# Performance work log

Hardware: AMD Instinct MI355X
Metric: run time of the kernel (lower is better)

Reference implementation:

```python
import jax, jax.numpy as jnp
import numpy as np

N_NODES = 100000
N_EDGES = 1600000
N_GRAPHS = 64
IN_DIM = 128
HID = 64
N_CLASSES = 10


def setup_inputs() -> dict:
    key = jax.random.key(0)
    ks = jax.random.split(key, 8)
    x = jax.random.normal(ks[0], (N_NODES, IN_DIM), jnp.float32)
    edge_index = jax.random.randint(ks[1], (2, N_EDGES), 0, N_NODES, jnp.int32)
    graph_id = jnp.sort(jax.random.randint(ks[2], (N_NODES,), 0, N_GRAPHS, jnp.int32))
    W1 = jax.random.normal(ks[3], (IN_DIM, HID), jnp.float32) / np.sqrt(IN_DIM)
    b1 = jnp.zeros((HID,), jnp.float32)
    W2 = jax.random.normal(ks[4], (HID, HID), jnp.float32) / np.sqrt(HID)
    b2 = jnp.zeros((HID,), jnp.float32)
    attn_W = jax.random.normal(ks[5], (HID, 1), jnp.float32) / np.sqrt(HID)
    attn_b = jnp.zeros((1,), jnp.float32)
    cls_W = jax.random.normal(ks[6], (HID, N_CLASSES), jnp.float32) / np.sqrt(HID)
    cls_b = jnp.zeros((N_CLASSES,), jnp.float32)
    return {"x": x, "edge_index": edge_index, "graph_id": graph_id,
            "W1": W1, "b1": b1, "W2": W2, "b2": b2,
            "attn_W": attn_W, "attn_b": attn_b, "cls_W": cls_W, "cls_b": cls_b}


def _graph_conv(h, W, b, src, dst, norm_out, norm_in):
    # DGL GraphConv, norm='both': D_in^{-1/2} A D_out^{-1/2} (h W) + b
    h = h @ W                                  # [N, out]
    h = h * norm_out[:, None]                  # scale by src out-degree^{-1/2}
    m = jax.ops.segment_sum(h[src], dst, num_segments=N_NODES)  # SpMM aggregation
    return m * norm_in[:, None] + b


def reference(x, edge_index, graph_id, W1, b1, W2, b2, attn_W, attn_b, cls_W, cls_b):
    src, dst = edge_index[0], edge_index[1]
    ones_e = jnp.ones((src.shape[0],), jnp.float32)
    deg_out = jnp.clip(jax.ops.segment_sum(ones_e, src, num_segments=N_NODES), 1.0)
    deg_in = jnp.clip(jax.ops.segment_sum(ones_e, dst, num_segments=N_NODES), 1.0)
    norm_out = jax.lax.rsqrt(deg_out)
    norm_in = jax.lax.rsqrt(deg_in)

    h = jax.nn.relu(_graph_conv(x, W1, b1, src, dst, norm_out, norm_in))
    h = jax.nn.relu(_graph_conv(h, W2, b2, src, dst, norm_out, norm_in))

    hw = jax.nn.sigmoid(h @ attn_W + attn_b)   # [N, 1] attention gate
    h = h * hw

    # mean_nodes: per-graph mean pooling
    sums = jax.ops.segment_sum(h, graph_id, num_segments=N_GRAPHS)        # [G, HID]
    cnts = jnp.clip(jax.ops.segment_sum(jnp.ones((N_NODES,), jnp.float32), graph_id,
                                        num_segments=N_GRAPHS), 1.0)
    hg = sums / cnts[:, None]
    out = hg @ cls_W + cls_b                   # [G, n_classes]
    return out, hw
```

## Files before the change

kernel.cpp:

```cpp
#include <hip/hip_runtime.h>
#include <stdint.h>


#define N_NODES   100000
#define N_EDGES   1600000
#define N_GRAPHS  64
#define IN_DIM    128
#define HID       64
#define N_CLASSES 10

#define NBUCK     391
#define P1B       196
#define EPB       8192
#define GB_BLOCKS 391
#define MTILES    6250
#define GEMM_BLOCKS 1563
#define NSLOT     (NBUCK * 256)
#define SPMM_BLOCKS 3128
#define POOL_SLICES 32
#define WS_NEED   33885952u

typedef __attribute__((ext_vector_type(8))) short short8v;
typedef __attribute__((ext_vector_type(4))) float f32x4;
typedef __bf16 bf16x8 __attribute__((ext_vector_type(8)));

__device__ __forceinline__ f32x4 mfma16(short8v a, short8v b, f32x4 c) {
  return __builtin_amdgcn_mfma_f32_16x16x32_bf16(
      __builtin_bit_cast(bf16x8, a), __builtin_bit_cast(bf16x8, b), c, 0, 0, 0);
}

__device__ __forceinline__ float bf2f(unsigned short u) {
  unsigned int v = ((unsigned int)u) << 16;
  float f;
  __builtin_memcpy(&f, &v, 4);
  return f;
}

__device__ __forceinline__ unsigned short f2bf(float f) {
  unsigned int x;
  __builtin_memcpy(&x, &f, 4);
  unsigned int lsb = (x >> 16) & 1u;
  x += 0x7fffu + lsb;
  return (unsigned short)(x >> 16);
}

__device__ __forceinline__ void unpack_bf2(unsigned int u, float& lo, float& hi) {
  unsigned int a = u << 16;
  unsigned int b = u & 0xffff0000u;
  __builtin_memcpy(&lo, &a, 4);
  __builtin_memcpy(&hi, &b, 4);
}

__device__ __forceinline__ float ldf(const void* p, int i, int mode) {
  return mode ? bf2f(((const unsigned short*)p)[i]) : ((const float*)p)[i];
}

__global__ __launch_bounds__(256) void fallback_kernel(unsigned short* __restrict__ out,
                                                       int n) {
  int i = blockIdx.x * 256 + threadIdx.x;
  if (i < n) out[i] = 0;
}

__global__ __launch_bounds__(256) void wcvt_kernel(
    const unsigned short* __restrict__ xu,
    const void* __restrict__ W1, const void* __restrict__ W2,
    const void* __restrict__ b1, const void* __restrict__ b2,
    const void* __restrict__ attnW, const void* __restrict__ attnb,
    const void* __restrict__ clsW, const void* __restrict__ clsb,
    unsigned short* __restrict__ W1hf, unsigned short* __restrict__ W1lf,
    unsigned short* __restrict__ W2hf, unsigned short* __restrict__ W2lf,
    float* __restrict__ b1f, float* __restrict__ b2f,
    float* __restrict__ attnWf, float* __restrict__ attnbf,
    float* __restrict__ clsWf, float* __restrict__ clsbf,
    int* __restrict__ flag) {
  __shared__ int cnt[4];
  __shared__ int smode;
  int tid = (int)threadIdx.x;
  unsigned u = xu[2 * tid];
  int e = (int)((u >> 7) & 0xFF);
  int ok = (e >= 110 && e <= 132) ? 1 : 0;
  unsigned long long m = __ballot(ok);
  if ((tid & 63) == 0) cnt[tid >> 6] = __popcll(m);
  __syncthreads();
  if (tid == 0) {
    smode = (cnt[0] + cnt[1] + cnt[2] + cnt[3] > 128) ? 1 : 0;
    if (blockIdx.x == 0) {
      flag[0] = smode;
      flag[1] = 1;
    }
  }
  __syncthreads();
  int mode = smode;

  int i = blockIdx.x * 256 + tid;
  if (i < 1024) {
    int tile = i >> 6, lane = i & 63;
    int kt = tile >> 2, ct = tile & 3;
#pragma unroll
    for (int j = 0; j < 8; ++j) {
      int k = kt * 32 + ((lane >> 4) << 3) + j;
      int d = (ct << 4) + (lane & 15);
      float v = ldf(W1, k * HID + d, mode);
      unsigned short h = f2bf(v);
      unsigned short l = f2bf(v - bf2f(h));
      W1hf[i * 8 + j] = h;
      W1lf[i * 8 + j] = l;
    }
  } else if (i < 1536) {
    int ii = i - 1024;
    int tile = ii >> 6, lane = ii & 63;
    int kt = tile >> 2, ct = tile & 3;
#pragma unroll
    for (int j = 0; j < 8; ++j) {
      int k = kt * 32 + ((lane >> 4) << 3) + j;
      int d = (ct << 4) + (lane & 15);
      float v = ldf(W2, k * HID + d, mode);
      unsigned short h = f2bf(v);
      unsigned short l = f2bf(v - bf2f(h));
      W2hf[ii * 8 + j] = h;
      W2lf[ii * 8 + j] = l;
    }
  }
  if (i < HID) {
    b1f[i] = ldf(b1, i, mode);
    b2f[i] = ldf(b2, i, mode);
    attnWf[i] = ldf(attnW, i, mode);
  }
  if (i == 0) attnbf[0] = ldf(attnb, 0, mode);
  if (i < HID * N_CLASSES) clsWf[i] = ldf(clsW, i, mode);
  if (i < N_CLASSES) clsbf[i] = ldf(clsb, i, mode);
}

template <int K, bool SCALE>
__device__ __forceinline__ void gemm_tile(
    const void* __restrict__ A, const unsigned short* __restrict__ Whf,
    const unsigned short* __restrict__ Wlf, const float* __restrict__ norm_out,
    unsigned short* __restrict__ out, int mode, int mtile, int lane) {
  int n0 = mtile << 4;
  int row = lane & 15;
  int kg = lane >> 4;
  f32x4 acc0 = {0.f, 0.f, 0.f, 0.f};
  f32x4 acc1 = {0.f, 0.f, 0.f, 0.f};
  f32x4 acc2 = {0.f, 0.f, 0.f, 0.f};
  f32x4 acc3 = {0.f, 0.f, 0.f, 0.f};
  const short8v* whb0 = (const short8v*)Whf + lane;
  const short8v* wlb0 = (const short8v*)Wlf + lane;
  if (mode) {
    const unsigned short* xr = (const unsigned short*)A + (size_t)(n0 + row) * K + (kg << 3);
#pragma unroll
    for (int kt = 0; kt < K / 32; ++kt) {
      uint4 va = *(const uint4*)(xr + kt * 32);
      short8v xh = __builtin_bit_cast(short8v, va);
      const short8v* wh = whb0 + (size_t)(kt * 4) * 64;
      const short8v* wl = wlb0 + (size_t)(kt * 4) * 64;
      acc0 = mfma16(xh, wh[0], acc0);
      acc1 = mfma16(xh, wh[64], acc1);
      acc2 = mfma16(xh, wh[128], acc2);
      acc3 = mfma16(xh, wh[192], acc3);
      acc0 = mfma16(xh, wl[0], acc0);
      acc1 = mfma16(xh, wl[64], acc1);
      acc2 = mfma16(xh, wl[128], acc2);
      acc3 = mfma16(xh, wl[192], acc3);
    }
  } else {
    const float* xr = (const float*)A + (size_t)(n0 + row) * K + (kg << 3);
#pragma unroll
    for (int kt = 0; kt < K / 32; ++kt) {
      float4 a0 = *(const float4*)(xr + kt * 32);
      float4 a1 = *(const float4*)(xr + kt * 32 + 4);
      float xv[8] = {a0.x, a0.y, a0.z, a0.w, a1.x, a1.y, a1.z, a1.w};
      short8v xh, xl;
#pragma unroll
      for (int j = 0; j < 8; ++j) {
        unsigned short h = f2bf(xv[j]);
        unsigned short l = f2bf(xv[j] - bf2f(h));
        xh[j] = (short)h;
        xl[j] = (short)l;
      }
      const short8v* wh = whb0 + (size_t)(kt * 4) * 64;
      const short8v* wl = wlb0 + (size_t)(kt * 4) * 64;
      acc0 = mfma16(xh, wh[0], acc0);
      acc1 = mfma16(xh, wh[64], acc1);
      acc2 = mfma16(xh, wh[128], acc2);
      acc3 = mfma16(xh, wh[192], acc3);
      acc0 = mfma16(xh, wl[0], acc0);
      acc1 = mfma16(xh, wl[64], acc1);
      acc2 = mfma16(xh, wl[128], acc2);
      acc3 = mfma16(xh, wl[192], acc3);
      acc0 = mfma16(xl, wh[0], acc0);
      acc1 = mfma16(xl, wh[64], acc1);
      acc2 = mfma16(xl, wh[128], acc2);
      acc3 = mfma16(xl, wh[192], acc3);
    }
  }
  int col = lane & 15;
#pragma unroll
  for (int i = 0; i < 4; ++i) {
    int n = n0 + (kg << 2) + i;
    float s = SCALE ? norm_out[n] : 1.f;
    size_t rb = (size_t)n << 6;
    out[rb + col]      = f2bf(acc0[i] * s);
    out[rb + 16 + col] = f2bf(acc1[i] * s);
    out[rb + 32 + col] = f2bf(acc2[i] * s);
    out[rb + 48 + col] = f2bf(acc3[i] * s);
  }
}

__global__ __launch_bounds__(256) void fatA_kernel(
    const int* __restrict__ ei, int* __restrict__ blkhistD,
    int* __restrict__ blkhistS,
    const int* __restrict__ gid, int* __restrict__ gstart,
    const void* __restrict__ x, const unsigned short* __restrict__ W1hf,
    const unsigned short* __restrict__ W1lf, unsigned short* __restrict__ bufA,
    const int* __restrict__ flag) {
  int b = (int)blockIdx.x;
  int t = (int)threadIdx.x;
  if (b < P1B) {
    __shared__ int hD[NBUCK];
    __shared__ int hS[NBUCK];
    for (int i = t; i < NBUCK; i += 256) { hD[i] = 0; hS[i] = 0; }
    __syncthreads();
    int base_e = b * EPB;
    for (int s = 0; s < EPB / 1024; ++s) {
      int e4 = base_e + s * 1024 + t * 4;
      if (e4 < N_EDGES) {
        int4 s4 = *(const int4*)(ei + e4);
        int4 d4 = *(const int4*)(ei + N_EDGES + e4);
        int ss[4] = {s4.x, s4.y, s4.z, s4.w};
        int dd[4] = {d4.x, d4.y, d4.z, d4.w};
#pragma unroll
        for (int j = 0; j < 4; ++j) {
          if ((unsigned)ss[j] < N_NODES) atomicAdd(&hS[ss[j] >> 8], 1);
          if ((unsigned)dd[j] < N_NODES) atomicAdd(&hD[dd[j] >> 8], 1);
        }
      }
    }
    __syncthreads();
    for (int i = t; i < NBUCK; i += 256) {
      blkhistD[i * P1B + b] = hD[i];
      blkhistS[i * P1B + b] = hS[i];
    }
  } else if (b < P1B + GEMM_BLOCKS) {
    int mode = flag[0];
    int mtile = (b - P1B) * 4 + (t >> 6);
    if (mtile < MTILES)
      gemm_tile<IN_DIM, false>(x, W1hf, W1lf, (const float*)0, bufA, mode,
                               mtile, t & 63);
  } else {
    int bb = b - P1B - GEMM_BLOCKS;
    int n = bb * 256 + t;
    if (n >= N_NODES) return;
    int gc = gid[n] & (N_GRAPHS - 1);
    if (n == 0) {
      for (int g = 0; g <= gc; ++g) gstart[g] = 0;
    } else {
      int gp = gid[n - 1] & (N_GRAPHS - 1);
      for (int g = gp + 1; g <= gc; ++g) gstart[g] = n;
    }
    if (n == N_NODES - 1) {
      for (int g = gc + 1; g <= N_GRAPHS; ++g) gstart[g] = N_NODES;
    }
  }
}

__global__ __launch_bounds__(512) void bucket_tot_kernel(
    const int* __restrict__ blkhistD, const int* __restrict__ blkhistS,
    int* __restrict__ bstart_d, int* __restrict__ bstart_s) {
  const int* hist = (blockIdx.x == 0) ? blkhistD : blkhistS;
  int* bst  = (blockIdx.x == 0) ? bstart_d : bstart_s;
  int u = (int)threadIdx.x;
  int tot = 0;
  if (u < NBUCK) {
    const int* row = hist + u * P1B;
    for (int blk = 0; blk < P1B; ++blk) tot += row[blk];
  }
  __shared__ int smA[512];
  __shared__ int smB[512];
  smA[u] = tot;
  __syncthreads();
  int* a = smA;
  int* bq = smB;
  for (int off = 1; off < 512; off <<= 1) {
    int v = a[u];
    if (u >= off) v += a[u - off];
    bq[u] = v;
    __syncthreads();
    int* tmp = a; a = bq; bq = tmp;
  }
  int excl = a[u] - tot;
  if (u <= NBUCK) bst[u] = excl;
}

__global__ __launch_bounds__(256) void bucket_base_kernel(
    int* __restrict__ blkhistD, int* __restrict__ blkhistS,
    const int* __restrict__ bstart_d, const int* __restrict__ bstart_s) {
  int bb = (int)blockIdx.x;
  int* hist = (bb < NBUCK) ? blkhistD : blkhistS;
  const int* bst = (bb < NBUCK) ? bstart_d : bstart_s;
  int u = (bb < NBUCK) ? bb : bb - NBUCK;
  int t = (int)threadIdx.x;
  int h = (t < P1B) ? hist[u * P1B + t] : 0;
  __shared__ int smA[256];
  __shared__ int smB[256];
  smA[t] = h;
  __syncthreads();
  int* a = smA;
  int* bq = smB;
  for (int off = 1; off < 256; off <<= 1) {
    int v = a[t];
    if (t >= off) v += a[t - off];
    bq[t] = v;
    __syncthreads();
    int* tmp = a; a = bq; bq = tmp;
  }
  int excl = a[t] - h;
  if (t < P1B) hist[u * P1B + t] = bst[u] + excl;
}

__global__ __launch_bounds__(256) void part_scatter_kernel(
    const int* __restrict__ ei, const int* __restrict__ blkbaseD,
    const int* __restrict__ blkbaseS,
    unsigned int* __restrict__ edstP, int* __restrict__ esrc) {
  __shared__ int cD[NBUCK];
  __shared__ int cS[NBUCK];
  int b = (int)blockIdx.x;
  int t = (int)threadIdx.x;
  for (int i = t; i < NBUCK; i += 256) {
    cD[i] = blkbaseD[i * P1B + b];
    cS[i] = blkbaseS[i * P1B + b];
  }
  __syncthreads();
  int base_e = b * EPB;
  for (int s = 0; s < EPB / 1024; ++s) {
    int e4 = base_e + s * 1024 + t * 4;
    if (e4 < N_EDGES) {
      int4 s4 = *(const int4*)(ei + e4);
      int4 d4 = *(const int4*)(ei + N_EDGES + e4);
      int ss[4] = {s4.x, s4.y, s4.z, s4.w};
      int dd[4] = {d4.x, d4.y, d4.z, d4.w};
#pragma unroll
      for (int j = 0; j < 4; ++j) {
        if ((unsigned)ss[j] < N_NODES) {
          int slot = atomicAdd(&cS[ss[j] >> 8], 1);
          esrc[slot] = ss[j];
        }
        if ((unsigned)dd[j] < N_NODES) {
          int slot = atomicAdd(&cD[dd[j] >> 8], 1);
          edstP[slot] = ((unsigned int)ss[j] << 8) | ((unsigned int)dd[j] & 255u);
        }
      }
    }
  }
}

__global__ __launch_bounds__(256) void csr_kernel(
    const unsigned int* __restrict__ edstP, const int* __restrict__ esrc,
    const int* __restrict__ bstart_d, const int* __restrict__ bstart_s,
    int* __restrict__ rowptr, int* __restrict__ colx,
    float* __restrict__ norm_in, float* __restrict__ norm_out,
    int* __restrict__ perm) {
  __shared__ int lc[256];
  __shared__ int smA[256];
  __shared__ int smB[256];
  int b = (int)blockIdx.x;
  int t = (int)threadIdx.x;
  if (b < NBUCK) {
    int node0 = b << 8;
    int base = bstart_d[b];
    int end  = bstart_d[b + 1];
    lc[t] = 0;
    __syncthreads();
    for (int i = base + t; i < end; i += 256) {
      unsigned int p = edstP[i];
      atomicAdd(&lc[p & 255u], 1);
    }
    __syncthreads();
    int my = lc[t];
    smA[t] = my;
    __syncthreads();
    int* a = smA;
    int* bq = smB;
    for (int off = 1; off < 256; off <<= 1) {
      int v = a[t];
      if (t >= off) v += a[t - off];
      bq[t] = v;
      __syncthreads();
      int* tmp = a; a = bq; bq = tmp;
    }
    int excl = a[t] - my;
    int n = node0 + t;
    if (n <= N_NODES) rowptr[n] = base + excl;
    if (n < N_NODES) {
      int c = my < 1 ? 1 : my;
      norm_in[n] = rsqrtf((float)c);
    }
    __syncthreads();
    lc[t] = base + excl;
    __syncthreads();
    for (int i = base + t; i < end; i += 256) {
      unsigned int p = edstP[i];
      int slot = atomicAdd(&lc[p & 255u], 1);
      colx[slot] = (int)(p >> 8);
    }
    __syncthreads();
    int deg = my < 255 ? my : 255;
    lc[t] = 0;
    __syncthreads();
    atomicAdd(&lc[deg], 1);
    __syncthreads();
    int hv = lc[t];
    smA[t] = hv;
    __syncthreads();
    int* a2 = smA;
    int* b2 = smB;
    for (int off = 1; off < 256; off <<= 1) {
      int v = a2[t];
      if (t >= off) v += a2[t - off];
      b2[t] = v;
      __syncthreads();
      int* tmp = a2; a2 = b2; b2 = tmp;
    }
    int hexcl = a2[t] - hv;
    __syncthreads();
    lc[t] = hexcl;
    __syncthreads();
    int rank = atomicAdd(&lc[deg], 1);
    perm[(b << 8) + rank] = n;
  } else {
    int bb = b - NBUCK;
    int node0 = bb << 8;
    int base = bstart_s[bb];
    int end  = bstart_s[bb + 1];
    lc[t] = 0;
    __syncthreads();
    for (int i = base + t; i < end; i += 256) {
      atomicAdd(&lc[esrc[i] - node0], 1);
    }
    __syncthreads();
    int n = node0 + t;
    if (n < N_NODES) {
      int c = lc[t] < 1 ? 1 : lc[t];
      norm_out[n] = rsqrtf((float)c);
    }
  }
}

template <int K>
__global__ __launch_bounds__(256) void gemm_mfma_kernel(
    const void* __restrict__ A, const unsigned short* __restrict__ Whf,
    const unsigned short* __restrict__ Wlf, const float* __restrict__ norm_out,
    unsigned short* __restrict__ out, const int* __restrict__ flag) {
  int mode = flag[0];
  int mtile = (int)blockIdx.x * 4 + ((int)threadIdx.x >> 6);
  if (mtile >= MTILES) return;
  gemm_tile<K, true>(A, Whf, Wlf, norm_out, out, mode, mtile,
                     (int)threadIdx.x & 63);
}

__device__ __forceinline__ void accum8f(uint4 v, float no, float acc[8]) {
  float lo, hi;
  unpack_bf2(v.x, lo, hi); acc[0] = fmaf(lo, no, acc[0]); acc[1] = fmaf(hi, no, acc[1]);
  unpack_bf2(v.y, lo, hi); acc[2] = fmaf(lo, no, acc[2]); acc[3] = fmaf(hi, no, acc[3]);
  unpack_bf2(v.z, lo, hi); acc[4] = fmaf(lo, no, acc[4]); acc[5] = fmaf(hi, no, acc[5]);
  unpack_bf2(v.w, lo, hi); acc[6] = fmaf(lo, no, acc[6]); acc[7] = fmaf(hi, no, acc[7]);
}

__device__ __forceinline__ void spmm_gather8s(const unsigned short* __restrict__ hs,
                                              const int* __restrict__ col,
                                              const float* __restrict__ no,
                                              int e0, int e1, int dim0,
                                              float acc[8]) {
  int e = e0;
  for (; e + 4 <= e1; e += 4) {
    int c0 = col[e], c1 = col[e + 1], c2 = col[e + 2], c3 = col[e + 3];
    float n0 = no[c0], n1 = no[c1], n2 = no[c2], n3 = no[c3];
    uint4 v0 = *(const uint4*)(hs + ((size_t)c0 << 6) + dim0);
    uint4 v1 = *(const uint4*)(hs + ((size_t)c1 << 6) + dim0);
    uint4 v2 = *(const uint4*)(hs + ((size_t)c2 << 6) + dim0);
    uint4 v3 = *(const uint4*)(hs + ((size_t)c3 << 6) + dim0);
    accum8f(v0, n0, acc);
    accum8f(v1, n1, acc);
    accum8f(v2, n2, acc);
    accum8f(v3, n3, acc);
  }
  for (; e < e1; ++e) {
    int c = col[e];
    uint4 v = *(const uint4*)(hs + ((size_t)c << 6) + dim0);
    accum8f(v, no[c], acc);
  }
}

__device__ __forceinline__ void accum8(uint4 v, float acc[8]) {
  float lo, hi;
  unpack_bf2(v.x, lo, hi); acc[0] += lo; acc[1] += hi;
  unpack_bf2(v.y, lo, hi); acc[2] += lo; acc[3] += hi;
  unpack_bf2(v.z, lo, hi); acc[4] += lo; acc[5] += hi;
  unpack_bf2(v.w, lo, hi); acc[6] += lo; acc[7] += hi;
}

__device__ __forceinline__ void spmm_gather8(const unsigned short* __restrict__ hs,
                                             const int* __restrict__ col,
                                             int e0, int e1, int dim0,
                                             float acc[8]) {
  int e = e0;
  for (; e + 4 <= e1; e += 4) {
    int c0 = col[e], c1 = col[e + 1], c2 = col[e + 2], c3 = col[e + 3];
    uint4 v0 = *(const uint4*)(hs + ((size_t)c0 << 6) + dim0);
    uint4 v1 = *(const uint4*)(hs + ((size_t)c1 << 6) + dim0);
    uint4 v2 = *(const uint4*)(hs + ((size_t)c2 << 6) + dim0);
    uint4 v3 = *(const uint4*)(hs + ((size_t)c3 << 6) + dim0);
    accum8(v0, acc);
    accum8(v1, acc);
    accum8(v2, acc);
    accum8(v3, acc);
  }
  for (; e < e1; ++e) {
    int c = col[e];
    uint4 v = *(const uint4*)(hs + ((size_t)c << 6) + dim0);
    accum8(v, acc);
  }
}

__global__ __launch_bounds__(256) void spmm_kernel(const unsigned short* __restrict__ hs,
                                                   const int* __restrict__ rowptr,
                                                   const int* __restrict__ col,
                                                   const float* __restrict__ norm_out,
                                                   const float* __restrict__ norm_in,
                                                   const float* __restrict__ b1f,
                                                   const int* __restrict__ perm,
                                                   unsigned short* __restrict__ out) {
  int slot = (int)(blockIdx.x * 32 + (threadIdx.x >> 3));
  int n = perm[slot];
  if ((unsigned)n >= N_NODES) return;
  int dim0 = ((int)threadIdx.x & 7) << 3;
  int e0 = rowptr[n], e1 = rowptr[n + 1];
  if (e0 < 0) e0 = 0;
  if (e1 > N_EDGES) e1 = N_EDGES;
  float acc[8];
#pragma unroll
  for (int i = 0; i < 8; ++i) acc[i] = 0.f;
  spmm_gather8s(hs, col, norm_out, e0, e1, dim0, acc);
  float nin = norm_in[n];
  unsigned int pk[4];
#pragma unroll
  for (int i = 0; i < 4; ++i) {
    float vlo = fmaxf(acc[2 * i] * nin + b1f[dim0 + 2 * i], 0.f);
    float vhi = fmaxf(acc[2 * i + 1] * nin + b1f[dim0 + 2 * i + 1], 0.f);
    pk[i] = (unsigned int)f2bf(vlo) | ((unsigned int)f2bf(vhi) << 16);
  }
  *(uint4*)(out + ((size_t)n << 6) + dim0) = make_uint4(pk[0], pk[1], pk[2], pk[3]);
}

__global__ __launch_bounds__(256) void spmm_attn_kernel(
    const unsigned short* __restrict__ hs,
    const int* __restrict__ rowptr, const int* __restrict__ col,
    const float* __restrict__ norm_in, const float* __restrict__ b2f,
    const float* __restrict__ attnWf, const float* __restrict__ attnbf,
    const int* __restrict__ perm,
    void* __restrict__ out_base, unsigned short* __restrict__ gated,
    const int* __restrict__ flag) {
  int mode = flag[0];
  int slot = (int)(blockIdx.x * 32 + (threadIdx.x >> 3));
  int n = perm[slot];
  if ((unsigned)n >= N_NODES) return;
  int dim0 = ((int)threadIdx.x & 7) << 3;
  int e0 = rowptr[n], e1 = rowptr[n + 1];
  if (e0 < 0) e0 = 0;
  if (e1 > N_EDGES) e1 = N_EDGES;
  float acc[8];
#pragma unroll
  for (int i = 0; i < 8; ++i) acc[i] = 0.f;
  spmm_gather8(hs, col, e0, e1, dim0, acc);
  float nin = norm_in[n];
  float vv[8];
  float p = 0.f;
#pragma unroll
  for (int i = 0; i < 8; ++i) {
    vv[i] = fmaxf(acc[i] * nin + b2f[dim0 + i], 0.f);
    p += vv[i] * attnWf[dim0 + i];
  }
#pragma unroll
  for (int m = 1; m <= 4; m <<= 1) p += __shfl_xor(p, m, 64);
  float logit = p + attnbf[0];
  float hwv = 1.f / (1.f + __expf(-logit));
  if ((threadIdx.x & 7) == 0) {
    if (mode) ((unsigned short*)out_base)[N_GRAPHS * N_CLASSES + n] = f2bf(hwv);
    else      ((float*)out_base)[N_GRAPHS * N_CLASSES + n] = hwv;
  }
  unsigned int pk[4];
#pragma unroll
  for (int i = 0; i < 4; ++i) {
    pk[i] = (unsigned int)f2bf(vv[2 * i] * hwv) |
            ((unsigned int)f2bf(vv[2 * i + 1] * hwv) << 16);
  }
  *(uint4*)(gated + ((size_t)n << 6) + dim0) = make_uint4(pk[0], pk[1], pk[2], pk[3]);
}

__global__ __launch_bounds__(256) void pool_kernel(const unsigned short* __restrict__ gated,
                                                   const int* __restrict__ gstart,
                                                   float* __restrict__ gpart) {
  int g = (int)blockIdx.x >> 5;
  int s = (int)blockIdx.x & 31;
  int dim = (int)threadIdx.x & 63;
  int rsel = (int)threadIdx.x >> 6;
  int r0 = gstart[g], r1 = gstart[g + 1];
  if (r0 < 0) r0 = 0;
  if (r1 > N_NODES) r1 = N_NODES;
  int len = r1 - r0;
  if (len < 0) len = 0;
  int a = r0 + (int)(((long long)len * s) >> 5);
  int bnd = r0 + (int)(((long long)len * (s + 1)) >> 5);
  float acc = 0.f;
  for (int r = a + rsel; r < bnd; r += 4)
    acc += bf2f(gated[((size_t)r << 6) + dim]);
  __shared__ float sm[256];
  sm[threadIdx.x] = acc;
  __syncthreads();
  if (threadIdx.x < 64)
    gpart[((size_t)blockIdx.x << 6) + dim] =
        sm[dim] + sm[64 + dim] + sm[128 + dim] + sm[192 + dim];
}

__global__ __launch_bounds__(640) void final_kernel(const float* __restrict__ gpart,
                                                    const int* __restrict__ gstart,
                                                    const float* __restrict__ clsWf,
                                                    const float* __restrict__ clsbf,
                                                    void* __restrict__ out_base,
                                                    const int* __restrict__ flag) {
  __shared__ float gs[N_GRAPHS * HID];
  int t = (int)threadIdx.x;
  for (int idx = t; idx < N_GRAPHS * HID; idx += 640) {
    int g = idx >> 6, d = idx & 63;
    float a = 0.f;
#pragma unroll
    for (int s = 0; s < POOL_SLICES; ++s)
      a += gpart[(((size_t)(g << 5) + s) << 6) + d];
    gs[idx] = a;
  }
  __syncthreads();
  int mode = flag[0];
  if (t >= N_GRAPHS * N_CLASSES) return;
  int g = t / N_CLASSES, c = t - g * N_CLASSES;
  int cg = gstart[g + 1] - gstart[g];
  if (cg < 1) cg = 1;
  float inv = 1.f / (float)cg;
  float acc = 0.f;
#pragma unroll
  for (int d = 0; d < HID; ++d) acc += gs[(g << 6) + d] * clsWf[d * N_CLASSES + c];
  float r = acc * inv + clsbf[c];
  if (mode) ((unsigned short*)out_base)[t] = f2bf(r);
  else      ((float*)out_base)[t] = r;
}

extern "C" void kernel_launch(void* const* d_in, const int* in_sizes, int n_in,
                              void* d_out, int out_size, void* d_ws, size_t ws_size,
                              hipStream_t stream) {
  const void* x     = d_in[0];
  const int*  ei    = (const int*)d_in[1];
  const int*  gid   = (const int*)d_in[2];
  const void* W1    = d_in[3];
  const void* b1    = d_in[4];
  const void* W2    = d_in[5];
  const void* b2    = d_in[6];
  const void* attnW = d_in[7];
  const void* attnb = d_in[8];
  const void* clsW  = d_in[9];
  const void* clsb  = d_in[10];

  if (ws_size < (size_t)WS_NEED) {
    fallback_kernel<<<(out_size + 255) / 256, 256, 0, stream>>>(
        (unsigned short*)d_out, out_size);
    return;
  }

  char* w = (char*)d_ws;
  int*   flag     = (int*)(w + 0);
  int*   gstart   = (int*)(w + 64);
  int*   bstart_d = (int*)(w + 16960);
  int*   bstart_s = (int*)(w + 18560);
  int*   blkhD    = (int*)(w + 20160);
  int*   blkhS    = (int*)(w + 326720);
  int*   rowptr   = (int*)(w + 633280);
  float* norm_out = (float*)(w + 1033344);
  float* norm_in  = (float*)(w + 1433344);
  unsigned short* W1hf = (unsigned short*)(w + 1833344);
  unsigned short* W1lf = (unsigned short*)(w + 1849728);
  unsigned short* W2hf = (unsigned short*)(w + 1866112);
  unsigned short* W2lf = (unsigned short*)(w + 1874304);
  float* b1f      = (float*)(w + 1882496);
  float* b2f      = (float*)(w + 1882752);
  float* attnWf   = (float*)(w + 1883008);
  float* attnbf   = (float*)(w + 1883264);
  float* clsWf    = (float*)(w + 1883328);
  float* clsbf    = (float*)(w + 1885888);
  int*   colx     = (int*)(w + 1885952);
  unsigned int* edstP = (unsigned int*)(w + 8285952);
  int*   esrc     = (int*)(w + 14685952);
  unsigned short* bufA = (unsigned short*)(w + 21085952);
  unsigned short* bufB = (unsigned short*)(w + 8285952);
  int*   perm     = (int*)(w + 20160);
  float* gpart    = (float*)(w + 20160);

  wcvt_kernel<<<32, 256, 0, stream>>>((const unsigned short*)x, W1, W2, b1, b2,
                                      attnW, attnb, clsW, clsb, W1hf, W1lf,
                                      W2hf, W2lf, b1f, b2f, attnWf, attnbf,
                                      clsWf, clsbf, flag);

  fatA_kernel<<<P1B + GEMM_BLOCKS + GB_BLOCKS, 256, 0, stream>>>(
      ei, blkhD, blkhS, gid, gstart, x, W1hf, W1lf, bufA, flag);

  bucket_tot_kernel<<<2, 512, 0, stream>>>(blkhD, blkhS, bstart_d, bstart_s);
  bucket_base_kernel<<<2 * NBUCK, 256, 0, stream>>>(blkhD, blkhS, bstart_d, bstart_s);

  part_scatter_kernel<<<P1B, 256, 0, stream>>>(ei, blkhD, blkhS, edstP, esrc);
  csr_kernel<<<2 * NBUCK, 256, 0, stream>>>(edstP, esrc, bstart_d, bstart_s,
                                            rowptr, colx, norm_in, norm_out, perm);

  spmm_kernel<<<SPMM_BLOCKS, 256, 0, stream>>>(bufA, rowptr, colx, norm_out,
                                               norm_in, b1f, perm, bufB);

  gemm_mfma_kernel<HID><<<GEMM_BLOCKS, 256, 0, stream>>>(
      bufB, W2hf, W2lf, norm_out, bufA, flag + 1);
  spmm_attn_kernel<<<SPMM_BLOCKS, 256, 0, stream>>>(
      bufA, rowptr, colx, norm_in, b2f, attnWf, attnbf, perm, d_out, bufB, flag);

  pool_kernel<<<N_GRAPHS * POOL_SLICES, 256, 0, stream>>>(bufB, gstart, gpart);
  final_kernel<<<1, 640, 0, stream>>>(gpart, gstart, clsWf, clsbf, d_out, flag);
}
```

Before: 287.7 us.

## Drop degree-sorted node permutation and deepen SpMM gather unroll to eight

Removes the per-bucket degree histogram, scan and permutation that csr_kernel built, so the SpMM kernels now map nodes directly by thread index instead of through perm. The gather loops are unrolled from four to eight edges, with all column loads issued before the feature loads to raise memory-level parallelism. This saves the sort work in csr_kernel and one indirection per SpMM row. It gives up the degree-balanced ordering within each 256-node bucket, so warps may see more load imbalance, and the wider unroll uses more registers.

```diff
diff --git a/kernel.cpp b/kernel.cpp
--- a/kernel.cpp
+++ b/kernel.cpp
@@ -15,8 +15,7 @@
 #define GB_BLOCKS 391
 #define MTILES    6250
 #define GEMM_BLOCKS 1563
-#define NSLOT     (NBUCK * 256)
-#define SPMM_BLOCKS 3128
+#define SPMM_BLOCKS 3125
 #define POOL_SLICES 32
 #define WS_NEED   33885952u
 
@@ -357,8 +356,7 @@
     const unsigned int* __restrict__ edstP, const int* __restrict__ esrc,
     const int* __restrict__ bstart_d, const int* __restrict__ bstart_s,
     int* __restrict__ rowptr, int* __restrict__ colx,
-    float* __restrict__ norm_in, float* __restrict__ norm_out,
-    int* __restrict__ perm) {
+    float* __restrict__ norm_in, float* __restrict__ norm_out) {
   __shared__ int lc[256];
   __shared__ int smA[256];
   __shared__ int smB[256];
@@ -402,30 +400,6 @@
       int slot = atomicAdd(&lc[p & 255u], 1);
       colx[slot] = (int)(p >> 8);
     }
-    __syncthreads();
-    int deg = my < 255 ? my : 255;
-    lc[t] = 0;
-    __syncthreads();
-    atomicAdd(&lc[deg], 1);
-    __syncthreads();
-    int hv = lc[t];
-    smA[t] = hv;
-    __syncthreads();
-    int* a2 = smA;
-    int* b2 = smB;
-    for (int off = 1; off < 256; off <<= 1) {
-      int v = a2[t];
-      if (t >= off) v += a2[t - off];
-      b2[t] = v;
-      __syncthreads();
-      int* tmp = a2; a2 = b2; b2 = tmp;
-    }
-    int hexcl = a2[t] - hv;
-    __syncthreads();
-    lc[t] = hexcl;
-    __syncthreads();
-    int rank = atomicAdd(&lc[deg], 1);
-    perm[(b << 8) + rank] = n;
   } else {
     int bb = b - NBUCK;
     int node0 = bb << 8;
@@ -471,17 +445,19 @@
                                               int e0, int e1, int dim0,
                                               float acc[8]) {
   int e = e0;
-  for (; e + 4 <= e1; e += 4) {
-    int c0 = col[e], c1 = col[e + 1], c2 = col[e + 2], c3 = col[e + 3];
-    float n0 = no[c0], n1 = no[c1], n2 = no[c2], n3 = no[c3];
-    uint4 v0 = *(const uint4*)(hs + ((size_t)c0 << 6) + dim0);
-    uint4 v1 = *(const uint4*)(hs + ((size_t)c1 << 6) + dim0);
-    uint4 v2 = *(const uint4*)(hs + ((size_t)c2 << 6) + dim0);
-    uint4 v3 = *(const uint4*)(hs + ((size_t)c3 << 6) + dim0);
-    accum8f(v0, n0, acc);
-    accum8f(v1, n1, acc);
-    accum8f(v2, n2, acc);
-    accum8f(v3, n3, acc);
+  for (; e + 8 <= e1; e += 8) {
+    int c[8];
+#pragma unroll
+    for (int j = 0; j < 8; ++j) c[j] = col[e + j];
+    uint4 v[8];
+#pragma unroll
+    for (int j = 0; j < 8; ++j)
+      v[j] = *(const uint4*)(hs + ((size_t)c[j] << 6) + dim0);
+    float nn[8];
+#pragma unroll
+    for (int j = 0; j < 8; ++j) nn[j] = no[c[j]];
+#pragma unroll
+    for (int j = 0; j < 8; ++j) accum8f(v[j], nn[j], acc);
   }
   for (; e < e1; ++e) {
     int c = col[e];
@@ -503,16 +479,16 @@
                                              int e0, int e1, int dim0,
                                              float acc[8]) {
   int e = e0;
-  for (; e + 4 <= e1; e += 4) {
-    int c0 = col[e], c1 = col[e + 1], c2 = col[e + 2], c3 = col[e + 3];
-    uint4 v0 = *(const uint4*)(hs + ((size_t)c0 << 6) + dim0);
-    uint4 v1 = *(const uint4*)(hs + ((size_t)c1 << 6) + dim0);
-    uint4 v2 = *(const uint4*)(hs + ((size_t)c2 << 6) + dim0);
-    uint4 v3 = *(const uint4*)(hs + ((size_t)c3 << 6) + dim0);
-    accum8(v0, acc);
-    accum8(v1, acc);
-    accum8(v2, acc);
-    accum8(v3, acc);
+  for (; e + 8 <= e1; e += 8) {
+    int c[8];
+#pragma unroll
+    for (int j = 0; j < 8; ++j) c[j] = col[e + j];
+    uint4 v[8];
+#pragma unroll
+    for (int j = 0; j < 8; ++j)
+      v[j] = *(const uint4*)(hs + ((size_t)c[j] << 6) + dim0);
+#pragma unroll
+    for (int j = 0; j < 8; ++j) accum8(v[j], acc);
   }
   for (; e < e1; ++e) {
     int c = col[e];
@@ -527,12 +503,10 @@
                                                    const float* __restrict__ norm_out,
                                                    const float* __restrict__ norm_in,
                                                    const float* __restrict__ b1f,
-                                                   const int* __restrict__ perm,
                                                    unsigned short* __restrict__ out) {
-  int slot = (int)(blockIdx.x * 32 + (threadIdx.x >> 3));
-  int n = perm[slot];
-  if ((unsigned)n >= N_NODES) return;
+  int n = (int)(blockIdx.x * 32 + (threadIdx.x >> 3));
   int dim0 = ((int)threadIdx.x & 7) << 3;
+  if (n >= N_NODES) return;
   int e0 = rowptr[n], e1 = rowptr[n + 1];
   if (e0 < 0) e0 = 0;
   if (e1 > N_EDGES) e1 = N_EDGES;
@@ -556,14 +530,12 @@
     const int* __restrict__ rowptr, const int* __restrict__ col,
     const float* __restrict__ norm_in, const float* __restrict__ b2f,
     const float* __restrict__ attnWf, const float* __restrict__ attnbf,
-    const int* __restrict__ perm,
     void* __restrict__ out_base, unsigned short* __restrict__ gated,
     const int* __restrict__ flag) {
   int mode = flag[0];
-  int slot = (int)(blockIdx.x * 32 + (threadIdx.x >> 3));
-  int n = perm[slot];
-  if ((unsigned)n >= N_NODES) return;
+  int n = (int)(blockIdx.x * 32 + (threadIdx.x >> 3));
   int dim0 = ((int)threadIdx.x & 7) << 3;
+  if (n >= N_NODES) return;
   int e0 = rowptr[n], e1 = rowptr[n + 1];
   if (e0 < 0) e0 = 0;
   if (e1 > N_EDGES) e1 = N_EDGES;
@@ -698,7 +670,6 @@
   int*   esrc     = (int*)(w + 14685952);
   unsigned short* bufA = (unsigned short*)(w + 21085952);
   unsigned short* bufB = (unsigned short*)(w + 8285952);
-  int*   perm     = (int*)(w + 20160);
   float* gpart    = (float*)(w + 20160);
 
   wcvt_kernel<<<32, 256, 0, stream>>>((const unsigned short*)x, W1, W2, b1, b2,
@@ -714,15 +685,15 @@
 
   part_scatter_kernel<<<P1B, 256, 0, stream>>>(ei, blkhD, blkhS, edstP, esrc);
   csr_kernel<<<2 * NBUCK, 256, 0, stream>>>(edstP, esrc, bstart_d, bstart_s,
-                                            rowptr, colx, norm_in, norm_out, perm);
+                                            rowptr, colx, norm_in, norm_out);
 
   spmm_kernel<<<SPMM_BLOCKS, 256, 0, stream>>>(bufA, rowptr, colx, norm_out,
-                                               norm_in, b1f, perm, bufB);
+                                               norm_in, b1f, bufB);
 
   gemm_mfma_kernel<HID><<<GEMM_BLOCKS, 256, 0, stream>>>(
       bufB, W2hf, W2lf, norm_out, bufA, flag + 1);
   spmm_attn_kernel<<<SPMM_BLOCKS, 256, 0, stream>>>(
-      bufA, rowptr, colx, norm_in, b2f, attnWf, attnbf, perm, d_out, bufB, flag);
+      bufA, rowptr, colx, norm_in, b2f, attnWf, attnbf, d_out, bufB, flag);
 
   pool_kernel<<<N_GRAPHS * POOL_SLICES, 256, 0, stream>>>(bufB, gstart, gpart);
   final_kernel<<<1, 640, 0, stream>>>(gpart, gstart, clsWf, clsbf, d_out, flag);
```

Result: faster. 280.7 us (-2.4%).
